# Performance work log

Hardware: AMD Instinct MI355X
Metric: run time of the kernel (lower is better)

## Reference

```python
import jax, jax.numpy as jnp
import numpy as np

N_NODES = 100000
D_IN = 128
D_HID = 256
N_EDGES = 3200000


def setup_inputs() -> dict:
    key = jax.random.key(0)
    k_x, k_e, k_w1, k_w2 = jax.random.split(key, 4)
    x = jax.random.normal(k_x, (N_NODES, D_IN), dtype=jnp.float32)
    edge_index = jax.random.randint(k_e, (2, N_EDGES), 0, N_NODES, dtype=jnp.int64)
    # Glorot-style init for GCN linear weights; PyG GCNConv has bias by default.
    W1 = jax.random.normal(k_w1, (D_IN, D_HID), dtype=jnp.float32) / np.sqrt(D_IN)
    b1 = jnp.zeros((D_HID,), dtype=jnp.float32)
    W2 = jax.random.normal(k_w2, (D_HID, D_HID), dtype=jnp.float32) / np.sqrt(D_HID)
    b2 = jnp.zeros((D_HID,), dtype=jnp.float32)
    return {"x": x, "edge_index": edge_index, "W1": W1, "b1": b1, "W2": W2, "b2": b2}


def gcn_conv(x, edge_index, W, b, num_nodes):
    # PyG GCNConv: add self-loops, symmetric normalization D^-1/2 A D^-1/2,
    # linear transform, scatter-add aggregation, bias.
    loop = jnp.arange(num_nodes, dtype=edge_index.dtype)
    src = jnp.concatenate([edge_index[0], loop])  # [E+N]
    dst = jnp.concatenate([edge_index[1], loop])  # [E+N]
    deg = jax.ops.segment_sum(jnp.ones_like(src, dtype=x.dtype), dst,
                              num_segments=num_nodes)  # in-degree incl. self-loop
    dinv = jnp.where(deg > 0, deg ** -0.5, 0.0)
    norm = dinv[src] * dinv[dst]  # [E+N]
    h = x @ W  # [N, D_out] -- transform before propagate (PyG order)
    msg = h[src] * norm[:, None]  # gather + scale: [E+N, D_out]
    out = jax.ops.segment_sum(msg, dst, num_segments=num_nodes)  # scatter-add
    return out + b


def reference(x, edge_index, W1, b1, W2, b2):
    n = x.shape[0]
    h = gcn_conv(x, edge_index, W1, b1, n)
    h = jax.nn.relu(h)
    # dropout is identity in eval mode (reference baseline runs deterministic)
    out = gcn_conv(h, edge_index, W2, b2, n)
    return out
```

## Files before the change

kernel.cpp:

```cpp
#include <hip/hip_runtime.h>


#define DF 256

typedef float f4v __attribute__((ext_vector_type(4)));
typedef short bf16x8 __attribute__((ext_vector_type(8)));
typedef float f32x4 __attribute__((ext_vector_type(4)));

__device__ inline void nt_store4(float* p, float4 v) {
  f4v t;
  t.x = v.x; t.y = v.y; t.z = v.z; t.w = v.w;
  __builtin_nontemporal_store(t, (f4v*)p);
}
__device__ inline unsigned short f2bf(float f) {
  unsigned u = __float_as_uint(f);
  return (unsigned short)((u + 0x7FFFu + ((u >> 16) & 1u)) >> 16);
}
__device__ inline float bf2f(unsigned short h) {
  return __uint_as_float(((unsigned)h) << 16);
}

__global__ __launch_bounds__(256) void zero_i32(int* __restrict__ p, int n) {
  int i = blockIdx.x * blockDim.x + threadIdx.x;
  if (i < n) p[i] = 0;
}

__global__ __launch_bounds__(256) void detect_kernel(const int* __restrict__ ei32,
                                                     int n_logical,
                                                     int* __restrict__ flag) {
  __shared__ int s_nonzero;
  if (threadIdx.x == 0) s_nonzero = 0;
  __syncthreads();
  const int n_half = n_logical >> 1;
  int step = n_half / 1024;
  if (step < 1) step = 1;
  for (int k = threadIdx.x; k < 1024; k += 256) {
    long idx = (long)k * step;
    if (idx < n_half && ei32[2 * idx + 1] != 0) atomicOr(&s_nonzero, 1);
  }
  __syncthreads();
  if (threadIdx.x == 0) flag[0] = s_nonzero ? 0 : 1;
}

__global__ __launch_bounds__(256) void convert_kernel(const int* __restrict__ ei32,
                                                      const int* __restrict__ flag,
                                                      int* __restrict__ conv, int n) {
  int i = blockIdx.x * blockDim.x + threadIdx.x;
  if (i < n) conv[i] = flag[0] ? ei32[2 * (size_t)i] : ei32[i];
}

__global__ __launch_bounds__(256) void xconv_kernel(const float* __restrict__ x,
                                                    unsigned short* __restrict__ xb,
                                                    int n8) {
  int i = blockIdx.x * blockDim.x + threadIdx.x;
  if (i < n8) {
    const float4 v0 = *(const float4*)&x[(size_t)i * 8];
    const float4 v1 = *(const float4*)&x[(size_t)i * 8 + 4];
    unsigned p0 = f2bf(v0.x) | ((unsigned)f2bf(v0.y) << 16);
    unsigned p1 = f2bf(v0.z) | ((unsigned)f2bf(v0.w) << 16);
    unsigned p2 = f2bf(v1.x) | ((unsigned)f2bf(v1.y) << 16);
    unsigned p3 = f2bf(v1.z) | ((unsigned)f2bf(v1.w) << 16);
    *(uint4*)&xb[(size_t)i * 8] = make_uint4(p0, p1, p2, p3);
  }
}

__global__ __launch_bounds__(256) void wconv_kernel(const float* __restrict__ W,
                                                    unsigned short* __restrict__ Wt, int K) {
  int idx = blockIdx.x * blockDim.x + threadIdx.x;
  if (idx < K * 256) {
    int k = idx / 256, c = idx % 256;
    Wt[c * K + k] = f2bf(W[idx]);
  }
}

__global__ __launch_bounds__(256) void count_kernel(const int* __restrict__ dst,
                                                    int* __restrict__ cnt, int E, int n) {
  int i = blockIdx.x * blockDim.x + threadIdx.x;
  if (i < E) {
    int d = dst[i];
    if ((unsigned)d < (unsigned)n) atomicAdd(&cnt[d], 1);
  }
}

__global__ __launch_bounds__(1024) void scan_kernel(const int* __restrict__ cnt,
                                                    int* __restrict__ row_ptr, int n) {
  __shared__ int wsum[16];
  __shared__ int s_base;
  const int tid = threadIdx.x;
  const int lane = tid & 63;
  const int wid = tid >> 6;
  if (tid == 0) s_base = 0;
  __syncthreads();
  for (int start = 0; start < n; start += 4096) {
    const int i0 = start + tid * 4;
    int v[4];
#pragma unroll
    for (int u = 0; u < 4; ++u) v[u] = (i0 + u < n) ? cnt[i0 + u] : 0;
    const int tsum = v[0] + v[1] + v[2] + v[3];
    int sc = tsum;
#pragma unroll
    for (int off = 1; off < 64; off <<= 1) {
      int t = __shfl_up(sc, off);
      if (lane >= off) sc += t;
    }
    if (lane == 63) wsum[wid] = sc;
    __syncthreads();
    if (wid == 0) {
      int ws = (lane < 16) ? wsum[lane] : 0;
#pragma unroll
      for (int off = 1; off < 16; off <<= 1) {
        int t = __shfl_up(ws, off);
        if (lane >= off) ws += t;
      }
      if (lane < 16) wsum[lane] = ws;
    }
    __syncthreads();
    int base = s_base + (wid > 0 ? wsum[wid - 1] : 0) + (sc - tsum);
#pragma unroll
    for (int u = 0; u < 4; ++u) {
      if (i0 + u < n) row_ptr[i0 + u] = base;
      base += v[u];
    }
    __syncthreads();
    if (tid == 1023) s_base += wsum[15];
    __syncthreads();
  }
  if (tid == 0) row_ptr[n] = s_base;
}

__global__ __launch_bounds__(256) void dinv_cursor_kernel(const int* __restrict__ cnt,
                                                          const int* __restrict__ row_ptr,
                                                          float* __restrict__ dinv,
                                                          int* __restrict__ cursor, int n) {
  int i = blockIdx.x * blockDim.x + threadIdx.x;
  if (i < n) {
    dinv[i] = rsqrtf((float)(cnt[i] + 1));
    cursor[i] = row_ptr[i];
  }
}

__global__ __launch_bounds__(256) void fill_kernel(const int* __restrict__ src,
                                                   const int* __restrict__ dst,
                                                   const float* __restrict__ dinv,
                                                   int* __restrict__ cursor,
                                                   int2* __restrict__ edge, int E, int n) {
  int i = blockIdx.x * blockDim.x + threadIdx.x;
  if (i < E) {
    int s = src[i], d = dst[i];
    if ((unsigned)s < (unsigned)n && (unsigned)d < (unsigned)n) {
      int pos = atomicAdd(&cursor[d], 1);
      edge[pos] = make_int2(s, __float_as_int(dinv[s] * dinv[d]));
    }
  }
}

template <int K, bool RELU, bool OBF16>
__global__ __launch_bounds__(256) void gemm_kernel(const float* __restrict__ X,
                                                   const unsigned short* __restrict__ Wt,
                                                   const float* __restrict__ bias,
                                                   void* __restrict__ outv, int M) {
  __shared__ unsigned short as_[32 * K];
  const int t = threadIdx.x;
  const int row0 = blockIdx.x * 32;

  for (int i = t; i < 4 * K; i += 256) {
    int r = i / (K / 8);
    int kk = (i % (K / 8)) * 8;
    int gr = row0 + r;
    float4 v0 = make_float4(0.f, 0.f, 0.f, 0.f), v1 = v0;
    if (gr < M) {
      v0 = *(const float4*)&X[(size_t)gr * K + kk];
      v1 = *(const float4*)&X[(size_t)gr * K + kk + 4];
    }
    unsigned p0 = f2bf(v0.x) | ((unsigned)f2bf(v0.y) << 16);
    unsigned p1 = f2bf(v0.z) | ((unsigned)f2bf(v0.w) << 16);
    unsigned p2 = f2bf(v1.x) | ((unsigned)f2bf(v1.y) << 16);
    unsigned p3 = f2bf(v1.z) | ((unsigned)f2bf(v1.w) << 16);
    unsigned byte = (unsigned)((r * K + kk) * 2) ^ ((unsigned)(r & 7) << 4);
    *(uint4*)((char*)as_ + byte) = make_uint4(p0, p1, p2, p3);
  }
  __syncthreads();

  const int l = t & 63;
  const int wv = t >> 6;
  const int lc = l & 15;
  const int lk = (l >> 4) * 8;

  f32x4 acc[2][4];
#pragma unroll
  for (int i = 0; i < 2; ++i)
#pragma unroll
    for (int j = 0; j < 4; ++j) acc[i][j] = (f32x4)0.f;

#pragma unroll
  for (int ks = 0; ks < K / 32; ++ks) {
    bf16x8 a[2];
#pragma unroll
    for (int mrep = 0; mrep < 2; ++mrep) {
      int row = mrep * 16 + lc;
      unsigned byte = (unsigned)((row * K + ks * 32 + lk) * 2) ^ ((unsigned)(row & 7) << 4);
      a[mrep] = *(const bf16x8*)((const char*)as_ + byte);
    }
    bf16x8 b[4];
#pragma unroll
    for (int nf = 0; nf < 4; ++nf) {
      int col = wv * 64 + nf * 16 + lc;
      b[nf] = *(const bf16x8*)&Wt[(size_t)col * K + ks * 32 + lk];
    }
#pragma unroll
    for (int mrep = 0; mrep < 2; ++mrep)
#pragma unroll
      for (int nf = 0; nf < 4; ++nf)
        acc[mrep][nf] = __builtin_amdgcn_mfma_f32_16x16x32_bf16(a[mrep], b[nf], acc[mrep][nf], 0, 0, 0);
  }

#pragma unroll
  for (int nf = 0; nf < 4; ++nf) {
    int gcol = wv * 64 + nf * 16 + lc;
    float bv = bias[gcol];
#pragma unroll
    for (int mrep = 0; mrep < 2; ++mrep) {
#pragma unroll
      for (int r = 0; r < 4; ++r) {
        int grow = row0 + mrep * 16 + (l >> 4) * 4 + r;
        if (grow < M) {
          float val = acc[mrep][nf][r] + bv;
          if (RELU) val = fmaxf(val, 0.f);
          if (OBF16)
            ((unsigned short*)outv)[(size_t)grow * DF + gcol] = f2bf(val);
          else
            ((float*)outv)[(size_t)grow * DF + gcol] = val;
        }
      }
    }
  }
}

__global__ __launch_bounds__(256) void agg256_kernel(const unsigned short* __restrict__ hb,
                                                     const int* __restrict__ row_ptr,
                                                     const int2* __restrict__ edge,
                                                     const float* __restrict__ dinv,
                                                     float* __restrict__ out, int n) {
  int wid = (blockIdx.x * blockDim.x + threadIdx.x) >> 6;
  int lane = threadIdx.x & 63;
  if (wid >= n) return;
  int start = row_ptr[wid];
  int end = row_ptr[wid + 1];
  const int foff = lane * 4;

  float4 acc = make_float4(0.f, 0.f, 0.f, 0.f);
  for (int base = start; base < end; base += 64) {
    int e = base + lane;
    int ce = 0;
    float we = 0.f;
    if (e < end) {
      long long ev = __builtin_nontemporal_load((const long long*)edge + e);
      ce = (int)(ev & 0xffffffffLL);
      we = __int_as_float((int)(ev >> 32));
    }
    int m = end - base;
    if (m > 64) m = 64;
    int j = 0;
    for (; j + 16 <= m; j += 16) {
      ushort4 hq[16];
      float ww[16];
#pragma unroll
      for (int u = 0; u < 16; ++u) {
        int s = __shfl(ce, j + u);
        ww[u] = __shfl(we, j + u);
        hq[u] = *(const ushort4*)&hb[(size_t)s * 256 + foff];
      }
#pragma unroll
      for (int u = 0; u < 16; ++u) {
        acc.x = fmaf(bf2f(hq[u].x), ww[u], acc.x);
        acc.y = fmaf(bf2f(hq[u].y), ww[u], acc.y);
        acc.z = fmaf(bf2f(hq[u].z), ww[u], acc.z);
        acc.w = fmaf(bf2f(hq[u].w), ww[u], acc.w);
      }
    }
    for (; j + 8 <= m; j += 8) {
      ushort4 hq[8];
      float ww[8];
#pragma unroll
      for (int u = 0; u < 8; ++u) {
        int s = __shfl(ce, j + u);
        ww[u] = __shfl(we, j + u);
        hq[u] = *(const ushort4*)&hb[(size_t)s * 256 + foff];
      }
#pragma unroll
      for (int u = 0; u < 8; ++u) {
        acc.x = fmaf(bf2f(hq[u].x), ww[u], acc.x);
        acc.y = fmaf(bf2f(hq[u].y), ww[u], acc.y);
        acc.z = fmaf(bf2f(hq[u].z), ww[u], acc.z);
        acc.w = fmaf(bf2f(hq[u].w), ww[u], acc.w);
      }
    }
    for (; j < m; ++j) {
      int s = __shfl(ce, j);
      float ww = __shfl(we, j);
      ushort4 hq = *(const ushort4*)&hb[(size_t)s * 256 + foff];
      acc.x = fmaf(bf2f(hq.x), ww, acc.x);
      acc.y = fmaf(bf2f(hq.y), ww, acc.y);
      acc.z = fmaf(bf2f(hq.z), ww, acc.z);
      acc.w = fmaf(bf2f(hq.w), ww, acc.w);
    }
  }
  float di = dinv[wid];
  float sw = di * di;
  ushort4 hq = *(const ushort4*)&hb[(size_t)wid * 256 + foff];
  acc.x = fmaf(bf2f(hq.x), sw, acc.x);
  acc.y = fmaf(bf2f(hq.y), sw, acc.y);
  acc.z = fmaf(bf2f(hq.z), sw, acc.z);
  acc.w = fmaf(bf2f(hq.w), sw, acc.w);
  nt_store4(&out[(size_t)wid * 256 + foff], acc);
}

__global__ __launch_bounds__(256) void agg128_kernel(const unsigned short* __restrict__ xb,
                                                     const int* __restrict__ row_ptr,
                                                     const int2* __restrict__ edge,
                                                     const float* __restrict__ dinv,
                                                     float* __restrict__ out, int n) {
  int wid = (blockIdx.x * blockDim.x + threadIdx.x) >> 6;
  int lane = threadIdx.x & 63;
  if (wid >= n) return;
  int start = row_ptr[wid];
  int end = row_ptr[wid + 1];
  const int half = lane >> 5;
  const int foff = (lane & 31) * 4;

  float4 acc = make_float4(0.f, 0.f, 0.f, 0.f);
  for (int base = start; base < end; base += 64) {
    int e = base + lane;
    int ce = 0;
    float we = 0.f;
    if (e < end) {
      long long ev = __builtin_nontemporal_load((const long long*)edge + e);
      ce = (int)(ev & 0xffffffffLL);
      we = __int_as_float((int)(ev >> 32));
    }
    int m = end - base;
    if (m > 64) m = 64;
    int j = 0;
    for (; j + 32 <= m; j += 32) {
      ushort4 hq[16];
      float ww[16];
#pragma unroll
      for (int u = 0; u < 16; ++u) {
        int idx = j + 2 * u + half;
        int s = __shfl(ce, idx);
        ww[u] = __shfl(we, idx);
        hq[u] = *(const ushort4*)&xb[(size_t)s * 128 + foff];
      }
#pragma unroll
      for (int u = 0; u < 16; ++u) {
        acc.x = fmaf(bf2f(hq[u].x), ww[u], acc.x);
        acc.y = fmaf(bf2f(hq[u].y), ww[u], acc.y);
        acc.z = fmaf(bf2f(hq[u].z), ww[u], acc.z);
        acc.w = fmaf(bf2f(hq[u].w), ww[u], acc.w);
      }
    }
    for (; j + 2 <= m; j += 2) {
      int idx = j + half;
      int s = __shfl(ce, idx);
      float ww = __shfl(we, idx);
      ushort4 hq = *(const ushort4*)&xb[(size_t)s * 128 + foff];
      acc.x = fmaf(bf2f(hq.x), ww, acc.x);
      acc.y = fmaf(bf2f(hq.y), ww, acc.y);
      acc.z = fmaf(bf2f(hq.z), ww, acc.z);
      acc.w = fmaf(bf2f(hq.w), ww, acc.w);
    }
    if (j < m) {
      int s = __shfl(ce, j);
      float ww = __shfl(we, j);
      if (half == 0) {
        ushort4 hq = *(const ushort4*)&xb[(size_t)s * 128 + foff];
        acc.x = fmaf(bf2f(hq.x), ww, acc.x);
        acc.y = fmaf(bf2f(hq.y), ww, acc.y);
        acc.z = fmaf(bf2f(hq.z), ww, acc.z);
        acc.w = fmaf(bf2f(hq.w), ww, acc.w);
      }
    }
  }
  acc.x += __shfl_xor(acc.x, 32);
  acc.y += __shfl_xor(acc.y, 32);
  acc.z += __shfl_xor(acc.z, 32);
  acc.w += __shfl_xor(acc.w, 32);
  if (half == 0) {
    float di = dinv[wid];
    float sw = di * di;
    ushort4 hq = *(const ushort4*)&xb[(size_t)wid * 128 + foff];
    acc.x = fmaf(bf2f(hq.x), sw, acc.x);
    acc.y = fmaf(bf2f(hq.y), sw, acc.y);
    acc.z = fmaf(bf2f(hq.z), sw, acc.z);
    acc.w = fmaf(bf2f(hq.w), sw, acc.w);
    nt_store4(&out[(size_t)wid * 128 + foff], acc);
  }
}

extern "C" void kernel_launch(void* const* d_in, const int* in_sizes, int n_in,
                              void* d_out, int out_size, void* d_ws, size_t ws_size,
                              hipStream_t stream) {
  const float* x = (const float*)d_in[0];
  const int* ei = (const int*)d_in[1];
  const float* W1 = (const float*)d_in[2];
  const float* b1 = (const float*)d_in[3];
  const float* W2 = (const float*)d_in[4];
  const float* b2 = (const float*)d_in[5];

  const int N = in_sizes[0] / 128;
  const int NE2 = in_sizes[1];
  const int E = NE2 / 2;

  char* p = (char*)d_ws;
  auto carve = [&](size_t bytes) {
    void* q = (void*)p;
    p += (bytes + 255) & ~(size_t)255;
    return q;
  };
  int* flag = (int*)carve(4);
  int* cnt = (int*)carve((size_t)N * 4);
  int* row_ptr = (int*)carve((size_t)(N + 1) * 4);
  int* cursor = (int*)carve((size_t)N * 4);
  float* dinv = (float*)carve((size_t)N * 4);
  int2* edge = (int2*)carve((size_t)E * 8);
  unsigned short* Wt1 = (unsigned short*)carve(128 * 256 * 2);
  unsigned short* Wt2 = (unsigned short*)carve(256 * 256 * 2);
  float* buf = (float*)carve((size_t)N * DF * 4);
  int* conv = (int*)buf;
  const int* src = conv;
  const int* dst = conv + E;
  unsigned short* hb = (unsigned short*)d_out;
  unsigned short* xb = (unsigned short*)((char*)d_out + (size_t)N * 256 * 2);

  detect_kernel<<<1, 256, 0, stream>>>(ei, NE2, flag);
  convert_kernel<<<(NE2 + 255) / 256, 256, 0, stream>>>(ei, flag, conv, NE2);
  xconv_kernel<<<(N * 128 / 8 + 255) / 256, 256, 0, stream>>>(x, xb, N * 128 / 8);
  wconv_kernel<<<(128 * 256 + 255) / 256, 256, 0, stream>>>(W1, Wt1, 128);
  wconv_kernel<<<(256 * 256 + 255) / 256, 256, 0, stream>>>(W2, Wt2, 256);

  zero_i32<<<(N + 255) / 256, 256, 0, stream>>>(cnt, N);
  count_kernel<<<(E + 255) / 256, 256, 0, stream>>>(dst, cnt, E, N);
  scan_kernel<<<1, 1024, 0, stream>>>(cnt, row_ptr, N);
  dinv_cursor_kernel<<<(N + 255) / 256, 256, 0, stream>>>(cnt, row_ptr, dinv, cursor, N);
  fill_kernel<<<(E + 255) / 256, 256, 0, stream>>>(src, dst, dinv, cursor, edge, E, N);

  const int agg_blocks = (N * 64 + 255) / 256;

  agg128_kernel<<<agg_blocks, 256, 0, stream>>>(xb, row_ptr, edge, dinv, buf, N);
  gemm_kernel<128, true, true><<<(N + 31) / 32, 256, 0, stream>>>(buf, Wt1, b1, hb, N);

  agg256_kernel<<<agg_blocks, 256, 0, stream>>>(hb, row_ptr, edge, dinv, buf, N);
  gemm_kernel<256, false, false><<<(N + 31) / 32, 256, 0, stream>>>(buf, Wt2, b2, d_out, N);
}
```

Measured before the change: 999.5 us.

## Fold symmetric normalization into node features and split 256-wide aggregation into halves

```diff
diff --git a/kernel.cpp b/kernel.cpp
--- a/kernel.cpp
+++ b/kernel.cpp
@@ -4,6 +4,7 @@
 #define DF 256
 
 typedef float f4v __attribute__((ext_vector_type(4)));
+typedef float f2v __attribute__((ext_vector_type(2)));
 typedef short bf16x8 __attribute__((ext_vector_type(8)));
 typedef float f32x4 __attribute__((ext_vector_type(4)));
 
@@ -11,6 +12,11 @@
   f4v t;
   t.x = v.x; t.y = v.y; t.z = v.z; t.w = v.w;
   __builtin_nontemporal_store(t, (f4v*)p);
+}
+__device__ inline void nt_store2(float* p, float a, float b) {
+  f2v t;
+  t.x = a; t.y = b;
+  __builtin_nontemporal_store(t, (f2v*)p);
 }
 __device__ inline unsigned short f2bf(float f) {
   unsigned u = __float_as_uint(f);
@@ -50,16 +56,18 @@
 }
 
 __global__ __launch_bounds__(256) void xconv_kernel(const float* __restrict__ x,
+                                                    const float* __restrict__ dinv,
                                                     unsigned short* __restrict__ xb,
                                                     int n8) {
   int i = blockIdx.x * blockDim.x + threadIdx.x;
   if (i < n8) {
+    float di = dinv[i / 16];
     const float4 v0 = *(const float4*)&x[(size_t)i * 8];
     const float4 v1 = *(const float4*)&x[(size_t)i * 8 + 4];
-    unsigned p0 = f2bf(v0.x) | ((unsigned)f2bf(v0.y) << 16);
-    unsigned p1 = f2bf(v0.z) | ((unsigned)f2bf(v0.w) << 16);
-    unsigned p2 = f2bf(v1.x) | ((unsigned)f2bf(v1.y) << 16);
-    unsigned p3 = f2bf(v1.z) | ((unsigned)f2bf(v1.w) << 16);
+    unsigned p0 = f2bf(di * v0.x) | ((unsigned)f2bf(di * v0.y) << 16);
+    unsigned p1 = f2bf(di * v0.z) | ((unsigned)f2bf(di * v0.w) << 16);
+    unsigned p2 = f2bf(di * v1.x) | ((unsigned)f2bf(di * v1.y) << 16);
+    unsigned p3 = f2bf(di * v1.z) | ((unsigned)f2bf(di * v1.w) << 16);
     *(uint4*)&xb[(size_t)i * 8] = make_uint4(p0, p1, p2, p3);
   }
 }
@@ -141,15 +149,14 @@
 
 __global__ __launch_bounds__(256) void fill_kernel(const int* __restrict__ src,
                                                    const int* __restrict__ dst,
-                                                   const float* __restrict__ dinv,
                                                    int* __restrict__ cursor,
-                                                   int2* __restrict__ edge, int E, int n) {
+                                                   int* __restrict__ col, int E, int n) {
   int i = blockIdx.x * blockDim.x + threadIdx.x;
   if (i < E) {
     int s = src[i], d = dst[i];
     if ((unsigned)s < (unsigned)n && (unsigned)d < (unsigned)n) {
       int pos = atomicAdd(&cursor[d], 1);
-      edge[pos] = make_int2(s, __float_as_int(dinv[s] * dinv[d]));
+      col[pos] = s;
     }
   }
 }
@@ -158,6 +165,7 @@
 __global__ __launch_bounds__(256) void gemm_kernel(const float* __restrict__ X,
                                                    const unsigned short* __restrict__ Wt,
                                                    const float* __restrict__ bias,
+                                                   const float* __restrict__ dinv,
                                                    void* __restrict__ outv, int M) {
   __shared__ unsigned short as_[32 * K];
   const int t = threadIdx.x;
@@ -226,19 +234,22 @@
         if (grow < M) {
           float val = acc[mrep][nf][r] + bv;
           if (RELU) val = fmaxf(val, 0.f);
-          if (OBF16)
+          if (OBF16) {
+            val *= dinv[grow];
             ((unsigned short*)outv)[(size_t)grow * DF + gcol] = f2bf(val);
-          else
+          } else {
             ((float*)outv)[(size_t)grow * DF + gcol] = val;
+          }
         }
       }
     }
   }
 }
 
+template <int HALF>
 __global__ __launch_bounds__(256) void agg256_kernel(const unsigned short* __restrict__ hb,
                                                      const int* __restrict__ row_ptr,
-                                                     const int2* __restrict__ edge,
+                                                     const int* __restrict__ col,
                                                      const float* __restrict__ dinv,
                                                      float* __restrict__ out, int n) {
   int wid = (blockIdx.x * blockDim.x + threadIdx.x) >> 6;
@@ -246,78 +257,44 @@
   if (wid >= n) return;
   int start = row_ptr[wid];
   int end = row_ptr[wid + 1];
-  const int foff = lane * 4;
-
-  float4 acc = make_float4(0.f, 0.f, 0.f, 0.f);
+  const int foff = HALF * 128 + lane * 2;
+
+  float ax = 0.f, ay = 0.f;
   for (int base = start; base < end; base += 64) {
     int e = base + lane;
     int ce = 0;
-    float we = 0.f;
-    if (e < end) {
-      long long ev = __builtin_nontemporal_load((const long long*)edge + e);
-      ce = (int)(ev & 0xffffffffLL);
-      we = __int_as_float((int)(ev >> 32));
-    }
+    if (e < end) ce = __builtin_nontemporal_load(&col[e]);
     int m = end - base;
     if (m > 64) m = 64;
     int j = 0;
     for (; j + 16 <= m; j += 16) {
-      ushort4 hq[16];
-      float ww[16];
+      ushort2 hq[16];
 #pragma unroll
       for (int u = 0; u < 16; ++u) {
         int s = __shfl(ce, j + u);
-        ww[u] = __shfl(we, j + u);
-        hq[u] = *(const ushort4*)&hb[(size_t)s * 256 + foff];
+        hq[u] = *(const ushort2*)&hb[(size_t)s * 256 + foff];
       }
 #pragma unroll
       for (int u = 0; u < 16; ++u) {
-        acc.x = fmaf(bf2f(hq[u].x), ww[u], acc.x);
-        acc.y = fmaf(bf2f(hq[u].y), ww[u], acc.y);
-        acc.z = fmaf(bf2f(hq[u].z), ww[u], acc.z);
-        acc.w = fmaf(bf2f(hq[u].w), ww[u], acc.w);
-      }
-    }
-    for (; j + 8 <= m; j += 8) {
-      ushort4 hq[8];
-      float ww[8];
-#pragma unroll
-      for (int u = 0; u < 8; ++u) {
-        int s = __shfl(ce, j + u);
-        ww[u] = __shfl(we, j + u);
-        hq[u] = *(const ushort4*)&hb[(size_t)s * 256 + foff];
-      }
-#pragma unroll
-      for (int u = 0; u < 8; ++u) {
-        acc.x = fmaf(bf2f(hq[u].x), ww[u], acc.x);
-        acc.y = fmaf(bf2f(hq[u].y), ww[u], acc.y);
-        acc.z = fmaf(bf2f(hq[u].z), ww[u], acc.z);
-        acc.w = fmaf(bf2f(hq[u].w), ww[u], acc.w);
+        ax += bf2f(hq[u].x);
+        ay += bf2f(hq[u].y);
       }
     }
     for (; j < m; ++j) {
       int s = __shfl(ce, j);
-      float ww = __shfl(we, j);
-      ushort4 hq = *(const ushort4*)&hb[(size_t)s * 256 + foff];
-      acc.x = fmaf(bf2f(hq.x), ww, acc.x);
-      acc.y = fmaf(bf2f(hq.y), ww, acc.y);
-      acc.z = fmaf(bf2f(hq.z), ww, acc.z);
-      acc.w = fmaf(bf2f(hq.w), ww, acc.w);
+      ushort2 hq = *(const ushort2*)&hb[(size_t)s * 256 + foff];
+      ax += bf2f(hq.x);
+      ay += bf2f(hq.y);
     }
   }
   float di = dinv[wid];
-  float sw = di * di;
-  ushort4 hq = *(const ushort4*)&hb[(size_t)wid * 256 + foff];
-  acc.x = fmaf(bf2f(hq.x), sw, acc.x);
-  acc.y = fmaf(bf2f(hq.y), sw, acc.y);
-  acc.z = fmaf(bf2f(hq.z), sw, acc.z);
-  acc.w = fmaf(bf2f(hq.w), sw, acc.w);
-  nt_store4(&out[(size_t)wid * 256 + foff], acc);
+  ushort2 own = *(const ushort2*)&hb[(size_t)wid * 256 + foff];
+  nt_store2(&out[(size_t)wid * 256 + foff], di * (ax + bf2f(own.x)), di * (ay + bf2f(own.y)));
 }
 
 __global__ __launch_bounds__(256) void agg128_kernel(const unsigned short* __restrict__ xb,
                                                      const int* __restrict__ row_ptr,
-                                                     const int2* __restrict__ edge,
+                                                     const int* __restrict__ col,
                                                      const float* __restrict__ dinv,
                                                      float* __restrict__ out, int n) {
   int wid = (blockIdx.x * blockDim.x + threadIdx.x) >> 6;
@@ -332,52 +309,41 @@
   for (int base = start; base < end; base += 64) {
     int e = base + lane;
     int ce = 0;
-    float we = 0.f;
-    if (e < end) {
-      long long ev = __builtin_nontemporal_load((const long long*)edge + e);
-      ce = (int)(ev & 0xffffffffLL);
-      we = __int_as_float((int)(ev >> 32));
-    }
+    if (e < end) ce = __builtin_nontemporal_load(&col[e]);
     int m = end - base;
     if (m > 64) m = 64;
     int j = 0;
     for (; j + 32 <= m; j += 32) {
       ushort4 hq[16];
-      float ww[16];
 #pragma unroll
       for (int u = 0; u < 16; ++u) {
-        int idx = j + 2 * u + half;
-        int s = __shfl(ce, idx);
-        ww[u] = __shfl(we, idx);
+        int s = __shfl(ce, j + 2 * u + half);
         hq[u] = *(const ushort4*)&xb[(size_t)s * 128 + foff];
       }
 #pragma unroll
       for (int u = 0; u < 16; ++u) {
-        acc.x = fmaf(bf2f(hq[u].x), ww[u], acc.x);
-        acc.y = fmaf(bf2f(hq[u].y), ww[u], acc.y);
-        acc.z = fmaf(bf2f(hq[u].z), ww[u], acc.z);
-        acc.w = fmaf(bf2f(hq[u].w), ww[u], acc.w);
+        acc.x += bf2f(hq[u].x);
+        acc.y += bf2f(hq[u].y);
+        acc.z += bf2f(hq[u].z);
+        acc.w += bf2f(hq[u].w);
       }
     }
     for (; j + 2 <= m; j += 2) {
-      int idx = j + half;
-      int s = __shfl(ce, idx);
-      float ww = __shfl(we, idx);
+      int s = __shfl(ce, j + half);
       ushort4 hq = *(const ushort4*)&xb[(size_t)s * 128 + foff];
-      acc.x = fmaf(bf2f(hq.x), ww, acc.x);
-      acc.y = fmaf(bf2f(hq.y), ww, acc.y);
-      acc.z = fmaf(bf2f(hq.z), ww, acc.z);
-      acc.w = fmaf(bf2f(hq.w), ww, acc.w);
+      acc.x += bf2f(hq.x);
+      acc.y += bf2f(hq.y);
+      acc.z += bf2f(hq.z);
+      acc.w += bf2f(hq.w);
     }
     if (j < m) {
       int s = __shfl(ce, j);
-      float ww = __shfl(we, j);
       if (half == 0) {
         ushort4 hq = *(const ushort4*)&xb[(size_t)s * 128 + foff];
-        acc.x = fmaf(bf2f(hq.x), ww, acc.x);
-        acc.y = fmaf(bf2f(hq.y), ww, acc.y);
-        acc.z = fmaf(bf2f(hq.z), ww, acc.z);
-        acc.w = fmaf(bf2f(hq.w), ww, acc.w);
+        acc.x += bf2f(hq.x);
+        acc.y += bf2f(hq.y);
+        acc.z += bf2f(hq.z);
+        acc.w += bf2f(hq.w);
       }
     }
   }
@@ -387,13 +353,13 @@
   acc.w += __shfl_xor(acc.w, 32);
   if (half == 0) {
     float di = dinv[wid];
-    float sw = di * di;
-    ushort4 hq = *(const ushort4*)&xb[(size_t)wid * 128 + foff];
-    acc.x = fmaf(bf2f(hq.x), sw, acc.x);
-    acc.y = fmaf(bf2f(hq.y), sw, acc.y);
-    acc.z = fmaf(bf2f(hq.z), sw, acc.z);
-    acc.w = fmaf(bf2f(hq.w), sw, acc.w);
-    nt_store4(&out[(size_t)wid * 128 + foff], acc);
+    ushort4 own = *(const ushort4*)&xb[(size_t)wid * 128 + foff];
+    float4 res;
+    res.x = di * (acc.x + bf2f(own.x));
+    res.y = di * (acc.y + bf2f(own.y));
+    res.z = di * (acc.z + bf2f(own.z));
+    res.w = di * (acc.w + bf2f(own.w));
+    nt_store4(&out[(size_t)wid * 128 + foff], res);
   }
 }
 
@@ -422,7 +388,7 @@
   int* row_ptr = (int*)carve((size_t)(N + 1) * 4);
   int* cursor = (int*)carve((size_t)N * 4);
   float* dinv = (float*)carve((size_t)N * 4);
-  int2* edge = (int2*)carve((size_t)E * 8);
+  int* col = (int*)carve((size_t)E * 4);
   unsigned short* Wt1 = (unsigned short*)carve(128 * 256 * 2);
   unsigned short* Wt2 = (unsigned short*)carve(256 * 256 * 2);
   float* buf = (float*)carve((size_t)N * DF * 4);
@@ -434,21 +400,22 @@
 
   detect_kernel<<<1, 256, 0, stream>>>(ei, NE2, flag);
   convert_kernel<<<(NE2 + 255) / 256, 256, 0, stream>>>(ei, flag, conv, NE2);
-  xconv_kernel<<<(N * 128 / 8 + 255) / 256, 256, 0, stream>>>(x, xb, N * 128 / 8);
-  wconv_kernel<<<(128 * 256 + 255) / 256, 256, 0, stream>>>(W1, Wt1, 128);
-  wconv_kernel<<<(256 * 256 + 255) / 256, 256, 0, stream>>>(W2, Wt2, 256);
-
   zero_i32<<<(N + 255) / 256, 256, 0, stream>>>(cnt, N);
   count_kernel<<<(E + 255) / 256, 256, 0, stream>>>(dst, cnt, E, N);
   scan_kernel<<<1, 1024, 0, stream>>>(cnt, row_ptr, N);
   dinv_cursor_kernel<<<(N + 255) / 256, 256, 0, stream>>>(cnt, row_ptr, dinv, cursor, N);
-  fill_kernel<<<(E + 255) / 256, 256, 0, stream>>>(src, dst, dinv, cursor, edge, E, N);
+  fill_kernel<<<(E + 255) / 256, 256, 0, stream>>>(src, dst, cursor, col, E, N);
+
+  xconv_kernel<<<(N * 128 / 8 + 255) / 256, 256, 0, stream>>>(x, dinv, xb, N * 128 / 8);
+  wconv_kernel<<<(128 * 256 + 255) / 256, 256, 0, stream>>>(W1, Wt1, 128);
+  wconv_kernel<<<(256 * 256 + 255) / 256, 256, 0, stream>>>(W2, Wt2, 256);
 
   const int agg_blocks = (N * 64 + 255) / 256;
 
-  agg128_kernel<<<agg_blocks, 256, 0, stream>>>(xb, row_ptr, edge, dinv, buf, N);
-  gemm_kernel<128, true, true><<<(N + 31) / 32, 256, 0, stream>>>(buf, Wt1, b1, hb, N);
-
-  agg256_kernel<<<agg_blocks, 256, 0, stream>>>(hb, row_ptr, edge, dinv, buf, N);
-  gemm_kernel<256, false, false><<<(N + 31) / 32, 256, 0, stream>>>(buf, Wt2, b2, d_out, N);
-}
+  agg128_kernel<<<agg_blocks, 256, 0, stream>>>(xb, row_ptr, col, dinv, buf, N);
+  gemm_kernel<128, true, true><<<(N + 31) / 32, 256, 0, stream>>>(buf, Wt1, b1, dinv, hb, N);
+
+  agg256_kernel<0><<<agg_blocks, 256, 0, stream>>>(hb, row_ptr, col, dinv, buf, N);
+  agg256_kernel<1><<<agg_blocks, 256, 0, stream>>>(hb, row_ptr, col, dinv, buf, N);
+  gemm_kernel<256, false, false><<<(N + 31) / 32, 256, 0, stream>>>(buf, Wt2, b2, dinv, d_out, N);
+}
```

Result: slower. 1.112 ms (+11.2%).
